# Kernel optimization log

Hardware: AMD Instinct MI355X
Metric: run time of the kernel (lower is better)

The kernel has to match this reference:

```python
import jax, jax.numpy as jnp
import numpy as np

N_NODES = 100000


def _sage_conv(x, src, dst, W_l, b_l, W_r):
    # mean-aggregate neighbor (source) features at target nodes
    gathered = x[src]                                   # [E, D]
    summed = jax.ops.segment_sum(gathered, dst, num_segments=N_NODES)  # [N, D]
    deg = jax.ops.segment_sum(jnp.ones((src.shape[0],), x.dtype), dst,
                              num_segments=N_NODES)     # [N]
    mean = summed / jnp.maximum(deg, 1.0)[:, None]      # zero stays zero for isolated nodes
    # PyG SAGEConv: lin_l(aggr) + lin_r(x); bias on lin_l only
    return mean @ W_l + b_l + x @ W_r


def setup_inputs() -> dict:
    key = jax.random.key(0)
    ks = jax.random.split(key, 9)
    x = jax.random.normal(ks[0], (N_NODES, 128), dtype=jnp.float32)
    edge_index = jax.random.randint(ks[1], (2, 1600000), 0, N_NODES, dtype=jnp.int64)
    s1 = 1.0 / np.sqrt(128.0)
    s2 = 1.0 / np.sqrt(32.0)
    return {
        "x": x,
        "edge_index": edge_index,
        "W1_l": jax.random.normal(ks[2], (128, 32), jnp.float32) * s1,
        "b1_l": jax.random.normal(ks[3], (32,), jnp.float32) * s1,
        "W1_r": jax.random.normal(ks[4], (128, 32), jnp.float32) * s1,
        "W2_l": jax.random.normal(ks[5], (32, 32), jnp.float32) * s2,
        "b2_l": jax.random.normal(ks[6], (32,), jnp.float32) * s2,
        "W2_r": jax.random.normal(ks[7], (32, 32), jnp.float32) * s2,
    }


def reference(x, edge_index, W1_l, b1_l, W1_r, W2_l, b2_l, W2_r):
    src, dst = edge_index[0], edge_index[1]
    h = _sage_conv(x, src, dst, W1_l, b1_l, W1_r)
    h = jax.nn.relu(h)
    # dropout is identity in eval mode
    h = _sage_conv(h, src, dst, W2_l, b2_l, W2_r)
    return jax.nn.relu(h)
```

## Files before the change

### kernel.cpp

```cpp
#include <hip/hip_runtime.h>


typedef _Float16 f16;
typedef _Float16 f16x2 __attribute__((ext_vector_type(2)));
typedef _Float16 f16x4 __attribute__((ext_vector_type(4)));
typedef _Float16 half8 __attribute__((ext_vector_type(8)));
typedef float f32x4 __attribute__((ext_vector_type(4)));

#define MAXBINS 2048
#define SHIFT 6
#define BINSZ 64
#define CAP 48
#define BSTR 52
#define GSC 256
#define BSC 512
#define SRC_BITS 17
#define SRC_MASK 0x1FFFFu
#define XSTRIDE 136


__global__ __launch_bounds__(256) void gemm_mfma(const float* __restrict__ x,
                                                 const float* __restrict__ Wl,
                                                 const float* __restrict__ Wr,
                                                 f16* __restrict__ yl,
                                                 float* __restrict__ yr,
                                                 int N) {
    __shared__ __align__(16) f16 sX[64 * XSTRIDE];
    __shared__ __align__(16) f16 sWT[64 * XSTRIDE];
    const int tid = threadIdx.x;
    const int row0 = blockIdx.x * 64;

    for (int i = tid; i < 64 * 32; i += 256) {
        int r = i >> 5, c4 = i & 31;
        int row = row0 + r;
        float4 v = make_float4(0.f, 0.f, 0.f, 0.f);
        if (row < N) v = *(const float4*)(x + (size_t)row * 128 + c4 * 4);
        f16* d = &sX[r * XSTRIDE + c4 * 4];
        d[0] = (f16)v.x; d[1] = (f16)v.y; d[2] = (f16)v.z; d[3] = (f16)v.w;
    }
    for (int i = tid; i < 64 * 128; i += 256) {
        int k = i >> 6, n = i & 63;
        float v = (n < 32) ? Wl[k * 32 + n] : Wr[k * 32 + (n - 32)];
        sWT[n * XSTRIDE + k] = (f16)v;
    }
    __syncthreads();

    const int w = tid >> 6;
    const int lane = tid & 63;
    const int l15 = lane & 15, quad = lane >> 4;
    f32x4 acc[4] = {};
#pragma unroll
    for (int kc = 0; kc < 4; ++kc) {
        half8 af = *(const half8*)&sX[(w * 16 + l15) * XSTRIDE + kc * 32 + quad * 8];
#pragma unroll
        for (int nt = 0; nt < 4; ++nt) {
            half8 bf = *(const half8*)&sWT[(nt * 16 + l15) * XSTRIDE + kc * 32 + quad * 8];
            acc[nt] = __builtin_amdgcn_mfma_f32_16x16x32_f16(af, bf, acc[nt], 0, 0, 0);
        }
    }
#pragma unroll
    for (int nt = 0; nt < 4; ++nt) {
        int c = nt * 16 + l15;
#pragma unroll
        for (int r = 0; r < 4; ++r) {
            int g = row0 + w * 16 + quad * 4 + r;
            if (c < 32) yl[(size_t)g * 32 + c] = (f16)acc[nt][r];
            else        yr[(size_t)g * 32 + (c - 32)] = acc[nt][r];
        }
    }
}


__global__ __launch_bounds__(BSC) void scatter_sort(const int* __restrict__ src,
                                                    const int* __restrict__ dst,
                                                    unsigned* __restrict__ pairs,
                                                    unsigned* __restrict__ binSeg,
                                                    int E, int chunk) {
    __shared__ int cnt[MAXBINS];
    __shared__ int wsum[8];
    const int tid = threadIdx.x;
    const int sb = blockIdx.x;
    for (int i = tid; i < MAXBINS; i += BSC) cnt[i] = 0;
    __syncthreads();

    const int base = sb * chunk;
    const int endE = base + chunk < E ? base + chunk : E;
    const int len = endE > base ? endE - base : 0;
    const int nv = len >> 2;
    const int rem = len & 3;
    const int4* s4 = (const int4*)(src + base);
    const int4* d4 = (const int4*)(dst + base);

    for (int i = tid; i < nv; i += BSC) {
        int4 d = d4[i];
        atomicAdd(&cnt[d.x >> SHIFT], 1);
        atomicAdd(&cnt[d.y >> SHIFT], 1);
        atomicAdd(&cnt[d.z >> SHIFT], 1);
        atomicAdd(&cnt[d.w >> SHIFT], 1);
    }
    if (tid < rem) atomicAdd(&cnt[dst[base + nv * 4 + tid] >> SHIFT], 1);
    __syncthreads();

    {
        int b0 = cnt[4 * tid], b1 = cnt[4 * tid + 1],
            b2 = cnt[4 * tid + 2], b3 = cnt[4 * tid + 3];
        int tsum = b0 + b1 + b2 + b3;
        const int lane = tid & 63, wave = tid >> 6;
        int incl = tsum;
#pragma unroll
        for (int off = 1; off < 64; off <<= 1) {
            int t = __shfl_up(incl, off, 64);
            if (lane >= off) incl += t;
        }
        if (lane == 63) wsum[wave] = incl;
        __syncthreads();
        if (tid == 0) {
            int a = 0;
#pragma unroll
            for (int w = 0; w < 8; ++w) { int t = wsum[w]; wsum[w] = a; a += t; }
        }
        __syncthreads();
        int ex = (incl - tsum) + wsum[wave];
        int e0 = ex, e1 = ex + b0, e2 = e1 + b1, e3 = e2 + b2;
        binSeg[(size_t)(4 * tid) * GSC + sb]     = ((unsigned)e0 << 16) | (unsigned)b0;
        binSeg[(size_t)(4 * tid + 1) * GSC + sb] = ((unsigned)e1 << 16) | (unsigned)b1;
        binSeg[(size_t)(4 * tid + 2) * GSC + sb] = ((unsigned)e2 << 16) | (unsigned)b2;
        binSeg[(size_t)(4 * tid + 3) * GSC + sb] = ((unsigned)e3 << 16) | (unsigned)b3;
        __syncthreads();
        cnt[4 * tid] = e0; cnt[4 * tid + 1] = e1;
        cnt[4 * tid + 2] = e2; cnt[4 * tid + 3] = e3;
    }
    __syncthreads();

    unsigned* out = pairs + (size_t)sb * chunk;
    for (int i = tid; i < nv; i += BSC) {
        int4 s = s4[i];
        int4 d = d4[i];
        int slot;
        slot = atomicAdd(&cnt[d.x >> SHIFT], 1);
        out[slot] = ((unsigned)(d.x & (BINSZ - 1)) << SRC_BITS) | (unsigned)s.x;
        slot = atomicAdd(&cnt[d.y >> SHIFT], 1);
        out[slot] = ((unsigned)(d.y & (BINSZ - 1)) << SRC_BITS) | (unsigned)s.y;
        slot = atomicAdd(&cnt[d.z >> SHIFT], 1);
        out[slot] = ((unsigned)(d.z & (BINSZ - 1)) << SRC_BITS) | (unsigned)s.z;
        slot = atomicAdd(&cnt[d.w >> SHIFT], 1);
        out[slot] = ((unsigned)(d.w & (BINSZ - 1)) << SRC_BITS) | (unsigned)s.w;
    }
    if (tid < rem) {
        int e = base + nv * 4 + tid;
        int s = src[e], d = dst[e];
        int slot = atomicAdd(&cnt[d >> SHIFT], 1);
        out[slot] = ((unsigned)(d & (BINSZ - 1)) << SRC_BITS) | (unsigned)s;
    }
}


__device__ __forceinline__ void build_bucket(const unsigned* __restrict__ pairs,
                                             const unsigned* __restrict__ binSeg,
                                             int* sBucket, int* sCnt,
                                             int b, int tid, int chunk) {
    unsigned dsc = binSeg[(size_t)b * GSC + tid];
    int scnt = (int)(dsc & 0xFFFFu);
    const unsigned* p = pairs + (size_t)tid * chunk + (dsc >> 16);
    int k = 0;
    for (; k + 4 <= scnt; k += 4) {
        unsigned p0 = p[k], p1 = p[k + 1], p2 = p[k + 2], p3 = p[k + 3];
        int l, s;
        l = p0 >> SRC_BITS; s = atomicAdd(&sCnt[l], 1);
        if (s < CAP) sBucket[l * BSTR + s] = (int)(p0 & SRC_MASK);
        l = p1 >> SRC_BITS; s = atomicAdd(&sCnt[l], 1);
        if (s < CAP) sBucket[l * BSTR + s] = (int)(p1 & SRC_MASK);
        l = p2 >> SRC_BITS; s = atomicAdd(&sCnt[l], 1);
        if (s < CAP) sBucket[l * BSTR + s] = (int)(p2 & SRC_MASK);
        l = p3 >> SRC_BITS; s = atomicAdd(&sCnt[l], 1);
        if (s < CAP) sBucket[l * BSTR + s] = (int)(p3 & SRC_MASK);
    }
    for (; k < scnt; ++k) {
        unsigned pk = p[k];
        int l = pk >> SRC_BITS;
        int s = atomicAdd(&sCnt[l], 1);
        if (s < CAP) sBucket[l * BSTR + s] = (int)(pk & SRC_MASK);
    }
}

#define PULL16(BKP, TBL, AX)                                                 \
    {                                                                        \
        int4 eA = (BKP)[0], eB = (BKP)[1], eC = (BKP)[2], eD = (BKP)[3];     \
        half8 v0 = *(const half8*)((TBL) + (size_t)eA.x * 32);               \
        half8 v1 = *(const half8*)((TBL) + (size_t)eA.y * 32);               \
        half8 v2 = *(const half8*)((TBL) + (size_t)eA.z * 32);               \
        half8 v3 = *(const half8*)((TBL) + (size_t)eA.w * 32);               \
        half8 v4 = *(const half8*)((TBL) + (size_t)eB.x * 32);               \
        half8 v5 = *(const half8*)((TBL) + (size_t)eB.y * 32);               \
        half8 v6 = *(const half8*)((TBL) + (size_t)eB.z * 32);               \
        half8 v7 = *(const half8*)((TBL) + (size_t)eB.w * 32);               \
        half8 v8 = *(const half8*)((TBL) + (size_t)eC.x * 32);               \
        half8 v9 = *(const half8*)((TBL) + (size_t)eC.y * 32);               \
        half8 va = *(const half8*)((TBL) + (size_t)eC.z * 32);               \
        half8 vb = *(const half8*)((TBL) + (size_t)eC.w * 32);               \
        half8 vc = *(const half8*)((TBL) + (size_t)eD.x * 32);               \
        half8 vd = *(const half8*)((TBL) + (size_t)eD.y * 32);               \
        half8 ve = *(const half8*)((TBL) + (size_t)eD.z * 32);               \
        half8 vf = *(const half8*)((TBL) + (size_t)eD.w * 32);               \
        _Pragma("unroll")                                                    \
        for (int k_ = 0; k_ < 8; ++k_)                                       \
            AX[k_] += ((((float)v0[k_] + (float)v1[k_]) +                    \
                        ((float)v2[k_] + (float)v3[k_])) +                   \
                       (((float)v4[k_] + (float)v5[k_]) +                    \
                        ((float)v6[k_] + (float)v7[k_]))) +                  \
                      ((((float)v8[k_] + (float)v9[k_]) +                    \
                        ((float)va[k_] + (float)vb[k_])) +                   \
                       (((float)vc[k_] + (float)vd[k_]) +                    \
                        ((float)ve[k_] + (float)vf[k_])));                   \
    }

__global__ __launch_bounds__(256, 4) void agg_l1(const unsigned* __restrict__ pairs,
                                                 const unsigned* __restrict__ binSeg,
                                                 const f16* __restrict__ yl,
                                                 const float* __restrict__ yr,
                                                 const float* __restrict__ b1,
                                                 const float* __restrict__ W2l,
                                                 const float* __restrict__ W2r,
                                                 f16* __restrict__ zl,
                                                 float* __restrict__ zr,
                                                 int N, int chunk) {
    __shared__ __align__(16) int sBucket[BINSZ * BSTR];
    __shared__ int sCnt[BINSZ];
    __shared__ __align__(16) float sW[2048];
    __shared__ __align__(16) float sB[32];
    const int tid = threadIdx.x;
    if (tid < BINSZ) sCnt[tid] = 0;
    if (tid < 32) sB[tid] = b1[tid];
    {
        float4* sW4 = (float4*)sW;
        sW4[tid] = ((const float4*)W2l)[tid];
        sW4[256 + tid] = ((const float4*)W2r)[tid];
        for (int i = tid; i < BINSZ * BSTR; i += 256) sBucket[i] = N;
    }
    __syncthreads();

    const int b = blockIdx.x;
    build_bucket(pairs, binSeg, sBucket, sCnt, b, tid, chunk);
    __syncthreads();

    const int node = tid >> 2;
    const int c8 = tid & 3;
    const int node0 = b << SHIFT;
    const int g = node0 + node;

    float4 locA = *(const float4*)(yr + (size_t)g * 32 + c8 * 8);
    float4 locB = *(const float4*)(yr + (size_t)g * 32 + c8 * 8 + 4);

    const int deg = sCnt[node];
    const int m = deg < CAP ? deg : CAP;
    const int q = (m + 15) >> 4;
    const int4* bk = (const int4*)&sBucket[node * BSTR];
    const f16* yb = yl + c8 * 8;

    float ax[8] = {0.f, 0.f, 0.f, 0.f, 0.f, 0.f, 0.f, 0.f};
    for (int j = 0; j < q; ++j) {
        PULL16(bk + 4 * j, yb, ax);
    }

    float h[8];
    if (g < N) {
        float dg = deg > 1 ? (float)deg : 1.0f;
        float loc[8];
        *(float4*)&loc[0] = locA;
        *(float4*)&loc[4] = locB;
#pragma unroll
        for (int k = 0; k < 8; ++k)
            h[k] = fmaxf(ax[k] / dg + sB[c8 * 8 + k] + loc[k], 0.0f);
    } else {
#pragma unroll
        for (int k = 0; k < 8; ++k) h[k] = 0.f;
    }
    __syncthreads();

    float* sH = (float*)sBucket;
    *(float4*)&sH[node * 36 + c8 * 8]     = make_float4(h[0], h[1], h[2], h[3]);
    *(float4*)&sH[node * 36 + c8 * 8 + 4] = make_float4(h[4], h[5], h[6], h[7]);
    __syncthreads();

    const int n2 = tid >> 3;
    const int cq = tid & 7;
    const float4* sW4l = (const float4*)sW;
    const float4* sW4r = (const float4*)(sW + 1024);
#pragma unroll
    for (int it = 0; it < 2; ++it) {
        int n = it * 32 + n2;
        int gg = node0 + n;
        float4 al = make_float4(0.f, 0.f, 0.f, 0.f);
        float4 ar = make_float4(0.f, 0.f, 0.f, 0.f);
#pragma unroll 8
        for (int k = 0; k < 32; ++k) {
            float hk = sH[n * 36 + k];
            float4 wl = sW4l[k * 8 + cq];
            float4 wr = sW4r[k * 8 + cq];
            al.x += hk * wl.x; al.y += hk * wl.y; al.z += hk * wl.z; al.w += hk * wl.w;
            ar.x += hk * wr.x; ar.y += hk * wr.y; ar.z += hk * wr.z; ar.w += hk * wr.w;
        }
        f16x4 hh;
        hh[0] = (f16)al.x; hh[1] = (f16)al.y; hh[2] = (f16)al.z; hh[3] = (f16)al.w;
        *(f16x4*)(zl + (size_t)gg * 32 + cq * 4) = hh;
        if (gg < N) *(float4*)(zr + (size_t)gg * 32 + cq * 4) = ar;
    }
}

__global__ __launch_bounds__(256, 4) void agg_l2(const unsigned* __restrict__ pairs,
                                                 const unsigned* __restrict__ binSeg,
                                                 const f16* __restrict__ zl,
                                                 const float* __restrict__ b2,
                                                 float* __restrict__ io,
                                                 int N, int chunk) {
    __shared__ __align__(16) int sBucket[BINSZ * BSTR];
    __shared__ int sCnt[BINSZ];
    __shared__ __align__(16) float sB[32];
    const int tid = threadIdx.x;
    if (tid < BINSZ) sCnt[tid] = 0;
    if (tid < 32) sB[tid] = b2[tid];
    for (int i = tid; i < BINSZ * BSTR; i += 256) sBucket[i] = N;
    __syncthreads();

    const int b = blockIdx.x;
    build_bucket(pairs, binSeg, sBucket, sCnt, b, tid, chunk);
    __syncthreads();

    const int node = tid >> 2;
    const int c8 = tid & 3;
    const int node0 = b << SHIFT;
    const int g = node0 + node;

    float4 ioA = make_float4(0.f, 0.f, 0.f, 0.f);
    float4 ioB = make_float4(0.f, 0.f, 0.f, 0.f);
    if (g < N) {
        ioA = *(const float4*)(io + (size_t)g * 32 + c8 * 8);
        ioB = *(const float4*)(io + (size_t)g * 32 + c8 * 8 + 4);
    }

    const int deg = sCnt[node];
    const int m = deg < CAP ? deg : CAP;
    const int q = (m + 15) >> 4;
    const int4* bk = (const int4*)&sBucket[node * BSTR];
    const f16* zb = zl + c8 * 8;

    float ax[8] = {0.f, 0.f, 0.f, 0.f, 0.f, 0.f, 0.f, 0.f};
    for (int j = 0; j < q; ++j) {
        PULL16(bk + 4 * j, zb, ax);
    }

    if (g < N) {
        float dg = deg > 1 ? (float)deg : 1.0f;
        float v[8];
        *(float4*)&v[0] = ioA;
        *(float4*)&v[4] = ioB;
        float o[8];
#pragma unroll
        for (int k = 0; k < 8; ++k)
            o[k] = fmaxf(ax[k] / dg + sB[c8 * 8 + k] + v[k], 0.0f);
        *(float4*)(io + (size_t)g * 32 + c8 * 8)     = *(float4*)&o[0];
        *(float4*)(io + (size_t)g * 32 + c8 * 8 + 4) = *(float4*)&o[4];
    }
}

extern "C" void kernel_launch(void* const* d_in, const int* in_sizes, int n_in,
                              void* d_out, int out_size, void* d_ws, size_t ws_size,
                              hipStream_t stream) {
    const float* x    = (const float*)d_in[0];
    const int*   ei   = (const int*)d_in[1];
    const float* W1l  = (const float*)d_in[2];
    const float* b1l  = (const float*)d_in[3];
    const float* W1r  = (const float*)d_in[4];
    const float* W2l  = (const float*)d_in[5];
    const float* b2l  = (const float*)d_in[6];
    const float* W2r  = (const float*)d_in[7];

    const int N = in_sizes[0] / 128;
    const int E = in_sizes[1] / 2;
    const int* srcIdx = ei;
    const int* dstIdx = ei + E;

    const int gridG = (N >> 6) + 1;
    const int NP = gridG << 6;

    const int nbins = (N + BINSZ - 1) >> SHIFT;
    const int chunk = (((E + GSC - 1) / GSC) + 3) & ~3;

    unsigned* binSeg = (unsigned*)d_ws;
    unsigned* pairs  = binSeg + (size_t)MAXBINS * GSC;
    f16*      A      = (f16*)(pairs + (size_t)GSC * chunk);
    float*    B      = (float*)(A + (size_t)NP * 32);
    f16*      Z      = (f16*)(B + (size_t)NP * 32);
    float*    outp   = (float*)d_out;

    gemm_mfma<<<gridG, 256, 0, stream>>>(x, W1l, W1r, A, B, N);
    scatter_sort<<<GSC, BSC, 0, stream>>>(srcIdx, dstIdx, pairs, binSeg, E, chunk);
    agg_l1<<<nbins, 256, 0, stream>>>(pairs, binSeg, A, B, b1l,
                                      W2l, W2r, Z, outp, N, chunk);
    agg_l2<<<nbins, 256, 0, stream>>>(pairs, binSeg, Z, b2l, outp, N, chunk);
}
```

Baseline: 196.9 us.

## Persist layer-1 neighbor buckets to global memory and reuse in layer 2

New measurement: 190.6 us. 1.03x faster.

```diff
diff --git a/kernel.cpp b/kernel.cpp
--- a/kernel.cpp
+++ b/kernel.cpp
@@ -2,7 +2,6 @@
 
 
 typedef _Float16 f16;
-typedef _Float16 f16x2 __attribute__((ext_vector_type(2)));
 typedef _Float16 f16x4 __attribute__((ext_vector_type(4)));
 typedef _Float16 half8 __attribute__((ext_vector_type(8)));
 typedef float f32x4 __attribute__((ext_vector_type(4)));
@@ -12,6 +11,7 @@
 #define BINSZ 64
 #define CAP 48
 #define BSTR 52
+#define GBI 3392
 #define GSC 256
 #define BSC 512
 #define SRC_BITS 17
@@ -183,39 +183,28 @@
     }
 }
 
-#define PULL16(BKP, TBL, AX)                                                 \
+#define PULL8(BKP, TBL, AX)                                                  \
     {                                                                        \
-        int4 eA = (BKP)[0], eB = (BKP)[1], eC = (BKP)[2], eD = (BKP)[3];     \
+        int4 eA = (BKP)[0], eB = (BKP)[1];                                   \
         half8 v0 = *(const half8*)((TBL) + (size_t)eA.x * 32);               \
         half8 v1 = *(const half8*)((TBL) + (size_t)eA.y * 32);               \
         half8 v2 = *(const half8*)((TBL) + (size_t)eA.z * 32);               \
         half8 v3 = *(const half8*)((TBL) + (size_t)eA.w * 32);               \
-        half8 v4 = *(const half8*)((TBL) + (size_t)eB.x * 32);               \
-        half8 v5 = *(const half8*)((TBL) + (size_t)eB.y * 32);               \
-        half8 v6 = *(const half8*)((TBL) + (size_t)eB.z * 32);               \
-        half8 v7 = *(const half8*)((TBL) + (size_t)eB.w * 32);               \
-        half8 v8 = *(const half8*)((TBL) + (size_t)eC.x * 32);               \
-        half8 v9 = *(const half8*)((TBL) + (size_t)eC.y * 32);               \
-        half8 va = *(const half8*)((TBL) + (size_t)eC.z * 32);               \
-        half8 vb = *(const half8*)((TBL) + (size_t)eC.w * 32);               \
-        half8 vc = *(const half8*)((TBL) + (size_t)eD.x * 32);               \
-        half8 vd = *(const half8*)((TBL) + (size_t)eD.y * 32);               \
-        half8 ve = *(const half8*)((TBL) + (size_t)eD.z * 32);               \
-        half8 vf = *(const half8*)((TBL) + (size_t)eD.w * 32);               \
+        half8 w0 = *(const half8*)((TBL) + (size_t)eB.x * 32);               \
+        half8 w1 = *(const half8*)((TBL) + (size_t)eB.y * 32);               \
+        half8 w2 = *(const half8*)((TBL) + (size_t)eB.z * 32);               \
+        half8 w3 = *(const half8*)((TBL) + (size_t)eB.w * 32);               \
         _Pragma("unroll")                                                    \
         for (int k_ = 0; k_ < 8; ++k_)                                       \
-            AX[k_] += ((((float)v0[k_] + (float)v1[k_]) +                    \
-                        ((float)v2[k_] + (float)v3[k_])) +                   \
-                       (((float)v4[k_] + (float)v5[k_]) +                    \
-                        ((float)v6[k_] + (float)v7[k_]))) +                  \
-                      ((((float)v8[k_] + (float)v9[k_]) +                    \
-                        ((float)va[k_] + (float)vb[k_])) +                   \
-                       (((float)vc[k_] + (float)vd[k_]) +                    \
-                        ((float)ve[k_] + (float)vf[k_])));                   \
+            AX[k_] += (((float)v0[k_] + (float)v1[k_]) +                     \
+                       ((float)v2[k_] + (float)v3[k_])) +                    \
+                      (((float)w0[k_] + (float)w1[k_]) +                     \
+                       ((float)w2[k_] + (float)w3[k_]));                     \
     }
 
 __global__ __launch_bounds__(256, 4) void agg_l1(const unsigned* __restrict__ pairs,
                                                  const unsigned* __restrict__ binSeg,
+                                                 int* __restrict__ gB,
                                                  const f16* __restrict__ yl,
                                                  const float* __restrict__ yr,
                                                  const float* __restrict__ b1,
@@ -225,7 +214,7 @@
                                                  float* __restrict__ zr,
                                                  int N, int chunk) {
     __shared__ __align__(16) int sBucket[BINSZ * BSTR];
-    __shared__ int sCnt[BINSZ];
+    __shared__ __align__(16) int sCnt[BINSZ];
     __shared__ __align__(16) float sW[2048];
     __shared__ __align__(16) float sB[32];
     const int tid = threadIdx.x;
@@ -243,6 +232,13 @@
     build_bucket(pairs, binSeg, sBucket, sCnt, b, tid, chunk);
     __syncthreads();
 
+    {
+        int4* g4 = (int4*)(gB + (size_t)b * GBI);
+        const int4* s4 = (const int4*)sBucket;
+        for (int i = tid; i < 832; i += 256) g4[i] = s4[i];
+        if (tid < 16) g4[832 + tid] = ((const int4*)sCnt)[tid];
+    }
+
     const int node = tid >> 2;
     const int c8 = tid & 3;
     const int node0 = b << SHIFT;
@@ -253,18 +249,18 @@
 
     const int deg = sCnt[node];
     const int m = deg < CAP ? deg : CAP;
-    const int q = (m + 15) >> 4;
+    const int q = (m + 7) >> 3;
     const int4* bk = (const int4*)&sBucket[node * BSTR];
-    const f16* yb = yl + c8 * 8;
+    const float dg = deg > 1 ? (float)deg : 1.0f;
 
     float ax[8] = {0.f, 0.f, 0.f, 0.f, 0.f, 0.f, 0.f, 0.f};
-    for (int j = 0; j < q; ++j) {
-        PULL16(bk + 4 * j, yb, ax);
+    {
+        const f16* yb = yl + c8 * 8;
+        for (int j = 0; j < q; ++j) PULL8(bk + 2 * j, yb, ax);
     }
 
     float h[8];
     if (g < N) {
-        float dg = deg > 1 ? (float)deg : 1.0f;
         float loc[8];
         *(float4*)&loc[0] = locA;
         *(float4*)&loc[4] = locB;
@@ -307,23 +303,24 @@
     }
 }
 
-__global__ __launch_bounds__(256, 4) void agg_l2(const unsigned* __restrict__ pairs,
-                                                 const unsigned* __restrict__ binSeg,
+__global__ __launch_bounds__(256, 4) void agg_l2(const int* __restrict__ gB,
                                                  const f16* __restrict__ zl,
                                                  const float* __restrict__ b2,
                                                  float* __restrict__ io,
-                                                 int N, int chunk) {
+                                                 int N) {
     __shared__ __align__(16) int sBucket[BINSZ * BSTR];
-    __shared__ int sCnt[BINSZ];
+    __shared__ __align__(16) int sCnt[BINSZ];
     __shared__ __align__(16) float sB[32];
     const int tid = threadIdx.x;
-    if (tid < BINSZ) sCnt[tid] = 0;
     if (tid < 32) sB[tid] = b2[tid];
-    for (int i = tid; i < BINSZ * BSTR; i += 256) sBucket[i] = N;
-    __syncthreads();
 
     const int b = blockIdx.x;
-    build_bucket(pairs, binSeg, sBucket, sCnt, b, tid, chunk);
+    {
+        const int4* g4 = (const int4*)(gB + (size_t)b * GBI);
+        int4* s4 = (int4*)sBucket;
+        for (int i = tid; i < 832; i += 256) s4[i] = g4[i];
+        if (tid < 16) ((int4*)sCnt)[tid] = g4[832 + tid];
+    }
     __syncthreads();
 
     const int node = tid >> 2;
@@ -340,13 +337,13 @@
 
     const int deg = sCnt[node];
     const int m = deg < CAP ? deg : CAP;
-    const int q = (m + 15) >> 4;
+    const int q = (m + 7) >> 3;
     const int4* bk = (const int4*)&sBucket[node * BSTR];
-    const f16* zb = zl + c8 * 8;
 
     float ax[8] = {0.f, 0.f, 0.f, 0.f, 0.f, 0.f, 0.f, 0.f};
-    for (int j = 0; j < q; ++j) {
-        PULL16(bk + 4 * j, zb, ax);
+    {
+        const f16* zb = zl + c8 * 8;
+        for (int j = 0; j < q; ++j) PULL8(bk + 2 * j, zb, ax);
     }
 
     if (g < N) {
@@ -391,11 +388,12 @@
     f16*      A      = (f16*)(pairs + (size_t)GSC * chunk);
     float*    B      = (float*)(A + (size_t)NP * 32);
     f16*      Z      = (f16*)(B + (size_t)NP * 32);
+    int*      gB     = (int*)(Z + (size_t)NP * 32);
     float*    outp   = (float*)d_out;
 
     gemm_mfma<<<gridG, 256, 0, stream>>>(x, W1l, W1r, A, B, N);
     scatter_sort<<<GSC, BSC, 0, stream>>>(srcIdx, dstIdx, pairs, binSeg, E, chunk);
-    agg_l1<<<nbins, 256, 0, stream>>>(pairs, binSeg, A, B, b1l,
+    agg_l1<<<nbins, 256, 0, stream>>>(pairs, binSeg, gB, A, B, b1l,
                                       W2l, W2r, Z, outp, N, chunk);
-    agg_l2<<<nbins, 256, 0, stream>>>(pairs, binSeg, Z, b2l, outp, N, chunk);
-}
+    agg_l2<<<nbins, 256, 0, stream>>>(gB, Z, b2l, outp, N);
+}
```
